# Performance work log

Hardware: AMD Instinct MI355X
Metric: run time of the kernel (lower is better)

## Reference

```python
import jax, jax.numpy as jnp
import numpy as np

WS = 8  # window_size; N = WS*WS = 64

def _rel_pos_index(ws):
    # identical to the torch buffer construction (meshgrid default 'ij')
    coords = np.stack(np.meshgrid(np.arange(ws), np.arange(ws), indexing='ij'))  # [2, ws, ws]
    cf = coords.reshape(2, -1)                       # [2, N]
    rel = cf[:, :, None] - cf[:, None, :]            # [2, N, N]
    rel = rel.transpose(1, 2, 0).astype(np.int64)    # [N, N, 2]
    rel[:, :, 0] += ws - 1
    rel[:, :, 1] += ws - 1
    rel[:, :, 0] *= 2 * ws - 1
    return jnp.asarray(rel.sum(-1), dtype=jnp.int32)  # [N, N] in [0, (2ws-1)^2)

def setup_inputs():
    key = jax.random.key(0)
    ks = jax.random.split(key, 4)
    B, N, C, H = 2048, WS * WS, 512, 16
    x = jax.random.normal(ks[0], (B, N, C), jnp.float32)
    qkv_w = jax.random.normal(ks[1], (C, 3 * C), jnp.float32) * 0.02
    proj_w = jax.random.normal(ks[2], (C, C), jnp.float32) * 0.02
    proj_b = jnp.zeros((C,), jnp.float32)
    bias_table = jax.random.normal(ks[3], ((2 * WS - 1) ** 2, H), jnp.float32) * 0.02
    rel_index = _rel_pos_index(WS)
    return {"x": x, "qkv_w": qkv_w, "proj_w": proj_w, "proj_b": proj_b,
            "bias_table": bias_table, "rel_index": rel_index}

def reference(x, qkv_w, proj_w, proj_b, bias_table, rel_index):
    B, N, C = x.shape
    H = bias_table.shape[1]
    d = C // H
    scale = d ** -0.5
    qkv = (x @ qkv_w).reshape(B, N, 3, H, d).transpose(2, 0, 3, 1, 4)  # [3,B,H,N,d]
    q, k, v = qkv[0], qkv[1], qkv[2]
    attn = jnp.einsum('bhnd,bhmd->bhnm', q, k) * scale                 # [B,H,N,N]
    bias = bias_table[rel_index.reshape(-1)].reshape(N, N, H).transpose(2, 0, 1)  # [H,N,N]
    attn = jax.nn.softmax(attn + bias[None], axis=-1)
    attn_map = attn  # dropout ratios are 0 / eval mode -> identity
    out = jnp.einsum('bhnm,bhmd->bhnd', attn, v).transpose(0, 2, 1, 3).reshape(B, N, C)
    out = out @ proj_w + proj_b
    return out, attn_map
```

## Files before the change

### kernel.cpp

```cpp
#include <hip/hip_runtime.h>
#include <cstdint>
#include <cstddef>

#define B_WIN   2048
#define N_TOK   64
#define C_DIM   512
#define H_HEADS 16
#define D_HEAD  32
#define K_DIM   512
#define M_ROWS  (B_WIN * 64)


typedef __bf16 bf16x8 __attribute__((ext_vector_type(8)));
typedef float  f32x4  __attribute__((ext_vector_type(4)));
typedef unsigned short u16x8 __attribute__((ext_vector_type(8)));

__device__ __forceinline__ unsigned short f2bf_rn(float f) {
    unsigned u = __float_as_uint(f);
    u += 0x7fffu + ((u >> 16) & 1u);
    return (unsigned short)(u >> 16);
}
__device__ __forceinline__ float bf2f(unsigned short h) {
    return __uint_as_float(((unsigned)h) << 16);
}
__device__ __forceinline__ void gload16(const void* g, void* l) {
    __builtin_amdgcn_global_load_lds(
        (const __attribute__((address_space(1))) void*)g,
        (__attribute__((address_space(3))) void*)l,
        16, 0, 0);
}

__global__ __launch_bounds__(256) void prep_kernel(
    const float* __restrict__ x,
    unsigned short* __restrict__ Xh,
    unsigned short* __restrict__ Xl,
    const float* __restrict__ qkv_w,
    unsigned short* __restrict__ qwTh,
    unsigned short* __restrict__ qwTl,
    const float* __restrict__ bias_table,
    const int* __restrict__ rel_index,
    float* __restrict__ bias_hn)
{
    const int blk = blockIdx.x;
    if (blk < 32768) {
        size_t e8 = ((size_t)blk * 256 + threadIdx.x) * 8;
        const int mb = (int)(e8 >> 16);
        const int w  = (int)(e8 & 65535);
        const int kt = w >> 12;
        const int s  = (w >> 10) & 3;
        const int r  = (w >> 3) & 127;
        const int m  = mb * 128 + r;
        const int k  = kt * 32 + s * 8;
        const float* src = &x[(size_t)m * 512 + k];
        float4 f0 = *reinterpret_cast<const float4*>(src);
        float4 f1 = *reinterpret_cast<const float4*>(src + 4);
        float fv[8] = {f0.x, f0.y, f0.z, f0.w, f1.x, f1.y, f1.z, f1.w};
        u16x8 hi, lo;
#pragma unroll
        for (int j = 0; j < 8; ++j) {
            unsigned short h = f2bf_rn(fv[j]);
            hi[j] = h;
            lo[j] = f2bf_rn(fv[j] - bf2f(h));
        }
        *reinterpret_cast<u16x8*>(&Xh[e8]) = hi;
        *reinterpret_cast<u16x8*>(&Xl[e8]) = lo;
    } else if (blk < 33152) {
        size_t e8 = ((size_t)(blk - 32768) * 256 + threadIdx.x) * 8;
        const int mb = (int)(e8 >> 16);
        const int ww = (int)(e8 & 65535);
        const int kt = ww >> 12;
        const int s  = (ww >> 10) & 3;
        const int r  = (ww >> 3) & 127;
        const int n  = mb * 128 + r;
        const int k  = kt * 32 + s * 8;
        u16x8 hi, lo;
#pragma unroll
        for (int j = 0; j < 8; ++j) {
            float v = qkv_w[(size_t)(k + j) * 1536 + n];
            unsigned short h = f2bf_rn(v);
            hi[j] = h;
            lo[j] = f2bf_rn(v - bf2f(h));
        }
        *reinterpret_cast<u16x8*>(&qwTh[e8]) = hi;
        *reinterpret_cast<u16x8*>(&qwTl[e8]) = lo;
    } else {
        int tid = (blk - 33152) * 256 + threadIdx.x;
        int h  = tid >> 12;
        int ij = tid & 4095;
        bias_hn[tid] = bias_table[rel_index[ij] * H_HEADS + h];
    }
}

__global__ __launch_bounds__(256) void wsplit_kernel(
    const float* __restrict__ w,
    unsigned short* __restrict__ wTh,
    unsigned short* __restrict__ wTl,
    int Ncols)
{
    size_t e8 = ((size_t)blockIdx.x * 256 + threadIdx.x) * 8;
    const int mb = (int)(e8 >> 16);
    const int ww = (int)(e8 & 65535);
    const int kt = ww >> 12;
    const int s  = (ww >> 10) & 3;
    const int r  = (ww >> 3) & 127;
    const int n  = mb * 128 + r;
    const int k  = kt * 32 + s * 8;
    u16x8 hi, lo;
#pragma unroll
    for (int j = 0; j < 8; ++j) {
        float v = w[(size_t)(k + j) * Ncols + n];
        unsigned short h = f2bf_rn(v);
        hi[j] = h;
        lo[j] = f2bf_rn(v - bf2f(h));
    }
    *reinterpret_cast<u16x8*>(&wTh[e8]) = hi;
    *reinterpret_cast<u16x8*>(&wTl[e8]) = lo;
}

__global__ __launch_bounds__(512, 2) void gemm_mfma_kernel(
    const unsigned short* __restrict__ ATh,
    const unsigned short* __restrict__ ATl,
    const unsigned short* __restrict__ BTh,
    const unsigned short* __restrict__ BTl,
    int mode,
    float* __restrict__ qkv_out,
    const float* __restrict__ bias,
    float* __restrict__ out,
    int Ncols_out,
    int nb_grid)
{
    extern __shared__ __align__(16) unsigned short L[];

    const int t    = threadIdx.x;
    const int lane = t & 63;
    const int wave = t >> 6;
    const int lg   = lane >> 4;
    const int lr   = lane & 15;
    const int wrow = (wave >> 2) * 128;
    const int wcol = (wave & 3) * 64;

    const int lin = blockIdx.x + gridDim.x * blockIdx.y;
    const int nwg = gridDim.x * gridDim.y;
    const int cpx = nwg >> 3;
    const int swz = (lin & 7) * cpx + (lin >> 3);
    const int m0  = (swz / nb_grid) * 256;
    const int n0  = (swz % nb_grid) * 256;
    const int mb0 = m0 >> 7;
    const int nb0 = n0 >> 7;

    f32x4 acc[8][4];
#pragma unroll
    for (int i = 0; i < 8; ++i)
#pragma unroll
        for (int j = 0; j < 4; ++j) acc[i][j] = (f32x4){0.f, 0.f, 0.f, 0.f};

    auto stage = [&](int kt, int bi) {
        const int bufbase = bi * 32768;
#pragma unroll
        for (int i = 0; i < 2; ++i) {
            const int c = i * 512 + t;
            const int r = c & 255;
            const int s = c >> 8;
            const size_t gA = (size_t)(mb0 + (r >> 7)) * 65536
                            + (size_t)kt * 4096 + s * 1024 + (r & 127) * 8;
            const size_t gB = (size_t)(nb0 + (r >> 7)) * 65536
                            + (size_t)kt * 4096 + s * 1024 + (r & 127) * 8;
            const int lo = bufbase + s * 2048 + r * 8;
            gload16(&ATh[gA], &L[lo]);
            gload16(&ATl[gA], &L[lo + 8192]);
            gload16(&BTh[gB], &L[lo + 16384]);
            gload16(&BTl[gB], &L[lo + 24576]);
        }
    };

    stage(0, 0);
    asm volatile("s_waitcnt vmcnt(0)" ::: "memory");
    __builtin_amdgcn_sched_barrier(0);
    __builtin_amdgcn_s_barrier();
    __builtin_amdgcn_sched_barrier(0);

#pragma unroll 2
    for (int ks = 0; ks < 16; ++ks) {
        const int cur = ks & 1;
        if (ks + 1 < 16) stage(ks + 1, cur ^ 1);
        const int bb = cur * 32768;

        bf16x8 bh[4], bl[4];
#pragma unroll
        for (int ni = 0; ni < 4; ++ni) {
            const int off = bb + lg * 2048 + (wcol + ni * 16 + lr) * 8;
            bh[ni] = *reinterpret_cast<const bf16x8*>(&L[off + 16384]);
            bl[ni] = *reinterpret_cast<const bf16x8*>(&L[off + 24576]);
        }
        __builtin_amdgcn_s_setprio(1);
#pragma unroll
        for (int mi = 0; mi < 8; ++mi) {
            const int aoff = bb + lg * 2048 + (wrow + mi * 16 + lr) * 8;
            bf16x8 ah = *reinterpret_cast<const bf16x8*>(&L[aoff]);
            bf16x8 al = *reinterpret_cast<const bf16x8*>(&L[aoff + 8192]);
#pragma unroll
            for (int ni = 0; ni < 4; ++ni)
                acc[mi][ni] = __builtin_amdgcn_mfma_f32_16x16x32_bf16(ah, bh[ni], acc[mi][ni], 0, 0, 0);
#pragma unroll
            for (int ni = 0; ni < 4; ++ni)
                acc[mi][ni] = __builtin_amdgcn_mfma_f32_16x16x32_bf16(ah, bl[ni], acc[mi][ni], 0, 0, 0);
#pragma unroll
            for (int ni = 0; ni < 4; ++ni)
                acc[mi][ni] = __builtin_amdgcn_mfma_f32_16x16x32_bf16(al, bh[ni], acc[mi][ni], 0, 0, 0);
        }
        __builtin_amdgcn_s_setprio(0);

        asm volatile("s_waitcnt vmcnt(0)" ::: "memory");
        __builtin_amdgcn_sched_barrier(0);
        __builtin_amdgcn_s_barrier();
        __builtin_amdgcn_sched_barrier(0);
    }

    if (mode == 0) {
#pragma unroll
        for (int mi = 0; mi < 8; ++mi)
#pragma unroll
            for (int ni = 0; ni < 4; ++ni) {
                const int col  = n0 + wcol + ni * 16 + lr;
                const int tsel = col >> 9;
                const int h    = (col >> 5) & 15;
                const int dd   = col & 31;
#pragma unroll
                for (int reg = 0; reg < 4; ++reg) {
                    const int row = m0 + wrow + mi * 16 + lg * 4 + reg;
                    const int b = row >> 6, n = row & 63;
                    qkv_out[((((size_t)tsel * B_WIN + b) * H_HEADS + h) * N_TOK + n) * D_HEAD + dd]
                        = acc[mi][ni][reg];
                }
            }
    } else {
#pragma unroll
        for (int mi = 0; mi < 8; ++mi)
#pragma unroll
            for (int ni = 0; ni < 4; ++ni) {
                const int col = n0 + wcol + ni * 16 + lr;
                const float pb = bias[col];
#pragma unroll
                for (int reg = 0; reg < 4; ++reg) {
                    const int row = m0 + wrow + mi * 16 + lg * 4 + reg;
                    out[(size_t)row * Ncols_out + col] = acc[mi][ni][reg] + pb;
                }
            }
    }
}

__global__ __launch_bounds__(256, 4) void attn_kernel(
    const float* __restrict__ qkv,
    const float* __restrict__ bias_hn,
    float* __restrict__ attn_map,
    unsigned short* __restrict__ avh,
    unsigned short* __restrict__ avl)
{
    __shared__ __align__(16) unsigned short SM[14848];
    constexpr int QH = 0, QL = 2560, KH = 5120, KL = 7680;
    constexpr int PH = 0, PL = 4608;
    constexpr int VTH = 10240, VTL = 12544;

    const int bh   = blockIdx.x;
    const int b    = bh >> 4;
    const int h    = bh & 15;
    const int t    = threadIdx.x;
    const int lane = t & 63;
    const int wv   = t >> 6;
    const int lg   = lane >> 4;
    const int lr   = lane & 15;

    const size_t plane = (size_t)B_WIN * H_HEADS * N_TOK * D_HEAD;
    const size_t base  = (size_t)bh * (N_TOK * D_HEAD);
    const float* qg = qkv + base;
    const float* kg = qkv + plane + base;
    const float* vg = qkv + 2 * plane + base;

    {
        const int r  = t >> 2;
        const int c0 = (t & 3) * 8;
        float4 a0 = *reinterpret_cast<const float4*>(&qg[r * 32 + c0]);
        float4 a1 = *reinterpret_cast<const float4*>(&qg[r * 32 + c0 + 4]);
        float qv[8] = {a0.x, a0.y, a0.z, a0.w, a1.x, a1.y, a1.z, a1.w};
        u16x8 hi, lo;
#pragma unroll
        for (int j = 0; j < 8; ++j) {
            unsigned short hh = f2bf_rn(qv[j]);
            hi[j] = hh; lo[j] = f2bf_rn(qv[j] - bf2f(hh));
        }
        *reinterpret_cast<u16x8*>(&SM[QH + r * 40 + c0]) = hi;
        *reinterpret_cast<u16x8*>(&SM[QL + r * 40 + c0]) = lo;

        float4 k0 = *reinterpret_cast<const float4*>(&kg[r * 32 + c0]);
        float4 k1 = *reinterpret_cast<const float4*>(&kg[r * 32 + c0 + 4]);
        float kv[8] = {k0.x, k0.y, k0.z, k0.w, k1.x, k1.y, k1.z, k1.w};
#pragma unroll
        for (int j = 0; j < 8; ++j) {
            unsigned short hh = f2bf_rn(kv[j]);
            hi[j] = hh; lo[j] = f2bf_rn(kv[j] - bf2f(hh));
        }
        *reinterpret_cast<u16x8*>(&SM[KH + r * 40 + c0]) = hi;
        *reinterpret_cast<u16x8*>(&SM[KL + r * 40 + c0]) = lo;

        float4 v0 = *reinterpret_cast<const float4*>(&vg[r * 32 + c0]);
        float4 v1 = *reinterpret_cast<const float4*>(&vg[r * 32 + c0 + 4]);
        float vv[8] = {v0.x, v0.y, v0.z, v0.w, v1.x, v1.y, v1.z, v1.w};
#pragma unroll
        for (int u = 0; u < 8; ++u) {
            const int d = c0 + u;
            unsigned short hh = f2bf_rn(vv[u]);
            SM[VTH + d * 72 + r] = hh;
            SM[VTL + d * 72 + r] = f2bf_rn(vv[u] - bf2f(hh));
        }
    }
    __syncthreads();

    float bias[4][4];
#pragma unroll
    for (int reg = 0; reg < 4; ++reg)
#pragma unroll
        for (int c = 0; c < 4; ++c)
            bias[reg][c] = bias_hn[(h << 12) + ((wv * 16 + lg * 4 + reg) << 6) + c * 16 + lr];

    const int ar = wv * 16 + lr;
    bf16x8 qa_h = *reinterpret_cast<const bf16x8*>(&SM[QH + ar * 40 + lg * 8]);
    bf16x8 qa_l = *reinterpret_cast<const bf16x8*>(&SM[QL + ar * 40 + lg * 8]);
    f32x4 S[4];
#pragma unroll
    for (int c = 0; c < 4; ++c) {
        const int br = c * 16 + lr;
        bf16x8 kb_h = *reinterpret_cast<const bf16x8*>(&SM[KH + br * 40 + lg * 8]);
        bf16x8 kb_l = *reinterpret_cast<const bf16x8*>(&SM[KL + br * 40 + lg * 8]);
        f32x4 s = (f32x4){0.f, 0.f, 0.f, 0.f};
        s = __builtin_amdgcn_mfma_f32_16x16x32_bf16(qa_h, kb_h, s, 0, 0, 0);
        s = __builtin_amdgcn_mfma_f32_16x16x32_bf16(qa_h, kb_l, s, 0, 0, 0);
        s = __builtin_amdgcn_mfma_f32_16x16x32_bf16(qa_l, kb_h, s, 0, 0, 0);
        S[c] = s;
    }
    __syncthreads();

    const float scale = 0.1767766952966369f;
    float p[4][4], mx[4], sm[4];
#pragma unroll
    for (int reg = 0; reg < 4; ++reg) mx[reg] = -1e30f;
#pragma unroll
    for (int reg = 0; reg < 4; ++reg)
#pragma unroll
        for (int c = 0; c < 4; ++c) {
            float s = fmaf(S[c][reg], scale, bias[reg][c]);
            p[reg][c] = s;
            mx[reg] = fmaxf(mx[reg], s);
        }
#pragma unroll
    for (int reg = 0; reg < 4; ++reg) {
        mx[reg] = fmaxf(mx[reg], __shfl_xor(mx[reg], 1));
        mx[reg] = fmaxf(mx[reg], __shfl_xor(mx[reg], 2));
        mx[reg] = fmaxf(mx[reg], __shfl_xor(mx[reg], 4));
        mx[reg] = fmaxf(mx[reg], __shfl_xor(mx[reg], 8));
        sm[reg] = 0.f;
    }
#pragma unroll
    for (int reg = 0; reg < 4; ++reg)
#pragma unroll
        for (int c = 0; c < 4; ++c) {
            float e = __expf(p[reg][c] - mx[reg]);
            p[reg][c] = e;
            sm[reg] += e;
        }
#pragma unroll
    for (int reg = 0; reg < 4; ++reg) {
        sm[reg] += __shfl_xor(sm[reg], 1);
        sm[reg] += __shfl_xor(sm[reg], 2);
        sm[reg] += __shfl_xor(sm[reg], 4);
        sm[reg] += __shfl_xor(sm[reg], 8);
        const float inv = 1.0f / sm[reg];
#pragma unroll
        for (int c = 0; c < 4; ++c) p[reg][c] *= inv;
    }

    const size_t amb = (size_t)bh * 4096;
#pragma unroll
    for (int reg = 0; reg < 4; ++reg) {
        const int R = wv * 16 + lg * 4 + reg;
#pragma unroll
        for (int c = 0; c < 4; ++c) {
            const int C = c * 16 + lr;
            const float own = p[reg][c];
            attn_map[amb + R * 64 + C] = own;
            const float mate = __shfl_xor(own, 1);
            if (!(lr & 1)) {
                unsigned short h0 = f2bf_rn(own);
                unsigned short l0 = f2bf_rn(own - bf2f(h0));
                unsigned short h1 = f2bf_rn(mate);
                unsigned short l1 = f2bf_rn(mate - bf2f(h1));
                *reinterpret_cast<unsigned*>(&SM[PH + R * 72 + C]) =
                    (unsigned)h0 | ((unsigned)h1 << 16);
                *reinterpret_cast<unsigned*>(&SM[PL + R * 72 + C]) =
                    (unsigned)l0 | ((unsigned)l1 << 16);
            }
        }
    }

    f32x4 O[2];
    O[0] = (f32x4){0.f, 0.f, 0.f, 0.f};
    O[1] = (f32x4){0.f, 0.f, 0.f, 0.f};
#pragma unroll
    for (int kk = 0; kk < 2; ++kk) {
        const int pr = wv * 16 + lr;
        bf16x8 pa_h = *reinterpret_cast<const bf16x8*>(&SM[PH + pr * 72 + kk * 32 + lg * 8]);
        bf16x8 pa_l = *reinterpret_cast<const bf16x8*>(&SM[PL + pr * 72 + kk * 32 + lg * 8]);
#pragma unroll
        for (int n = 0; n < 2; ++n) {
            const int vr = n * 16 + lr;
            bf16x8 vb_h = *reinterpret_cast<const bf16x8*>(&SM[VTH + vr * 72 + kk * 32 + lg * 8]);
            bf16x8 vb_l = *reinterpret_cast<const bf16x8*>(&SM[VTL + vr * 72 + kk * 32 + lg * 8]);
            O[n] = __builtin_amdgcn_mfma_f32_16x16x32_bf16(pa_h, vb_h, O[n], 0, 0, 0);
            O[n] = __builtin_amdgcn_mfma_f32_16x16x32_bf16(pa_h, vb_l, O[n], 0, 0, 0);
            O[n] = __builtin_amdgcn_mfma_f32_16x16x32_bf16(pa_l, vb_h, O[n], 0, 0, 0);
        }
    }

    const int mb = b >> 1;
#pragma unroll
    for (int n = 0; n < 2; ++n)
#pragma unroll
        for (int reg = 0; reg < 4; ++reg) {
            const int R  = wv * 16 + lg * 4 + reg;
            const int d  = n * 16 + lr;
            const int rl = (b & 1) * 64 + R;
            const float o = O[n][reg];
            unsigned short oh = f2bf_rn(o);
            unsigned short ol = f2bf_rn(o - bf2f(oh));
            size_t off = (size_t)mb * 65536 + (size_t)h * 4096
                       + (size_t)(d >> 3) * 1024 + (size_t)rl * 8 + (d & 7);
            avh[off] = oh;
            avl[off] = ol;
        }
}

extern "C" void kernel_launch(void* const* d_in, const int* in_sizes, int n_in,
                              void* d_out, int out_size, void* d_ws, size_t ws_size,
                              hipStream_t stream) {
    const float* x          = (const float*)d_in[0];
    const float* qkv_w      = (const float*)d_in[1];
    const float* proj_w     = (const float*)d_in[2];
    const float* proj_b     = (const float*)d_in[3];
    const float* bias_table = (const float*)d_in[4];
    const int*   rel_index  = (const int*)d_in[5];

    float* out      = (float*)d_out;
    float* attn_map = (float*)d_out + (size_t)M_ROWS * C_DIM;

    unsigned short* Xh  = (unsigned short*)d_ws;
    unsigned short* Xl  = Xh + (size_t)M_ROWS * 512;
    float*          qkv = (float*)(Xl + (size_t)M_ROWS * 512);
    unsigned short* avh = Xh;
    unsigned short* avl = Xl;

    unsigned short* qwTh = (unsigned short*)attn_map;
    unsigned short* qwTl = qwTh + (size_t)1536 * 512;
    unsigned short* pwTh = (unsigned short*)qkv;
    unsigned short* pwTl = pwTh + (size_t)512 * 512;
    float* bias_hn = out;

    prep_kernel<<<33408, 256, 0, stream>>>(
        x, Xh, Xl, qkv_w, qwTh, qwTl, bias_table, rel_index, bias_hn);
    gemm_mfma_kernel<<<dim3(6, 512), 512, 131072, stream>>>(
        Xh, Xl, qwTh, qwTl, 0, qkv, nullptr, nullptr, 1536, 6);
    attn_kernel<<<B_WIN * H_HEADS, 256, 0, stream>>>(
        qkv, bias_hn, attn_map, avh, avl);
    wsplit_kernel<<<128, 256, 0, stream>>>(proj_w, pwTh, pwTl, 512);
    gemm_mfma_kernel<<<dim3(2, 512), 512, 131072, stream>>>(
        avh, avl, pwTh, pwTl, 1, nullptr, proj_b, out, 512, 2);
}
```

Before: 1.179 ms.

## Store QKV as bf16 and drop split-precision passes in QK and projection

```diff
diff --git a/kernel.cpp b/kernel.cpp
--- a/kernel.cpp
+++ b/kernel.cpp
@@ -117,19 +117,27 @@
     *reinterpret_cast<u16x8*>(&wTl[e8]) = lo;
 }
 
+template<int NPASS>
 __global__ __launch_bounds__(512, 2) void gemm_mfma_kernel(
     const unsigned short* __restrict__ ATh,
     const unsigned short* __restrict__ ATl,
     const unsigned short* __restrict__ BTh,
     const unsigned short* __restrict__ BTl,
-    int mode,
-    float* __restrict__ qkv_out,
+    unsigned short* __restrict__ qh,
+    unsigned short* __restrict__ kh,
+    unsigned short* __restrict__ vh,
+    unsigned short* __restrict__ vl,
     const float* __restrict__ bias,
     float* __restrict__ out,
     int Ncols_out,
     int nb_grid)
 {
     extern __shared__ __align__(16) unsigned short L[];
+    constexpr int AH = 0;
+    constexpr int AL = 8192;
+    constexpr int BH = (NPASS == 3) ? 16384 : 8192;
+    constexpr int BL = (NPASS == 3) ? 24576 : 16384;
+    constexpr int STRIDE = (NPASS == 3) ? 32768 : 24576;
 
     const int t    = threadIdx.x;
     const int lane = t & 63;
@@ -155,7 +163,7 @@
         for (int j = 0; j < 4; ++j) acc[i][j] = (f32x4){0.f, 0.f, 0.f, 0.f};
 
     auto stage = [&](int kt, int bi) {
-        const int bufbase = bi * 32768;
+        const int bufbase = bi * STRIDE;
 #pragma unroll
         for (int i = 0; i < 2; ++i) {
             const int c = i * 512 + t;
@@ -166,10 +174,10 @@
             const size_t gB = (size_t)(nb0 + (r >> 7)) * 65536
                             + (size_t)kt * 4096 + s * 1024 + (r & 127) * 8;
             const int lo = bufbase + s * 2048 + r * 8;
-            gload16(&ATh[gA], &L[lo]);
-            gload16(&ATl[gA], &L[lo + 8192]);
-            gload16(&BTh[gB], &L[lo + 16384]);
-            gload16(&BTl[gB], &L[lo + 24576]);
+            gload16(&ATh[gA], &L[lo + AH]);
+            if constexpr (NPASS == 3) gload16(&ATl[gA], &L[lo + AL]);
+            gload16(&BTh[gB], &L[lo + BH]);
+            gload16(&BTl[gB], &L[lo + BL]);
         }
     };
 
@@ -183,30 +191,32 @@
     for (int ks = 0; ks < 16; ++ks) {
         const int cur = ks & 1;
         if (ks + 1 < 16) stage(ks + 1, cur ^ 1);
-        const int bb = cur * 32768;
+        const int bb = cur * STRIDE;
 
         bf16x8 bh[4], bl[4];
 #pragma unroll
         for (int ni = 0; ni < 4; ++ni) {
             const int off = bb + lg * 2048 + (wcol + ni * 16 + lr) * 8;
-            bh[ni] = *reinterpret_cast<const bf16x8*>(&L[off + 16384]);
-            bl[ni] = *reinterpret_cast<const bf16x8*>(&L[off + 24576]);
+            bh[ni] = *reinterpret_cast<const bf16x8*>(&L[off + BH]);
+            bl[ni] = *reinterpret_cast<const bf16x8*>(&L[off + BL]);
         }
         __builtin_amdgcn_s_setprio(1);
 #pragma unroll
         for (int mi = 0; mi < 8; ++mi) {
             const int aoff = bb + lg * 2048 + (wrow + mi * 16 + lr) * 8;
-            bf16x8 ah = *reinterpret_cast<const bf16x8*>(&L[aoff]);
-            bf16x8 al = *reinterpret_cast<const bf16x8*>(&L[aoff + 8192]);
+            bf16x8 ah = *reinterpret_cast<const bf16x8*>(&L[aoff + AH]);
 #pragma unroll
             for (int ni = 0; ni < 4; ++ni)
                 acc[mi][ni] = __builtin_amdgcn_mfma_f32_16x16x32_bf16(ah, bh[ni], acc[mi][ni], 0, 0, 0);
 #pragma unroll
             for (int ni = 0; ni < 4; ++ni)
                 acc[mi][ni] = __builtin_amdgcn_mfma_f32_16x16x32_bf16(ah, bl[ni], acc[mi][ni], 0, 0, 0);
-#pragma unroll
-            for (int ni = 0; ni < 4; ++ni)
-                acc[mi][ni] = __builtin_amdgcn_mfma_f32_16x16x32_bf16(al, bh[ni], acc[mi][ni], 0, 0, 0);
+            if constexpr (NPASS == 3) {
+                bf16x8 al = *reinterpret_cast<const bf16x8*>(&L[aoff + AL]);
+#pragma unroll
+                for (int ni = 0; ni < 4; ++ni)
+                    acc[mi][ni] = __builtin_amdgcn_mfma_f32_16x16x32_bf16(al, bh[ni], acc[mi][ni], 0, 0, 0);
+            }
         }
         __builtin_amdgcn_s_setprio(0);
 
@@ -216,7 +226,7 @@
         __builtin_amdgcn_sched_barrier(0);
     }
 
-    if (mode == 0) {
+    if constexpr (NPASS == 3) {
 #pragma unroll
         for (int mi = 0; mi < 8; ++mi)
 #pragma unroll
@@ -229,8 +239,17 @@
                 for (int reg = 0; reg < 4; ++reg) {
                     const int row = m0 + wrow + mi * 16 + lg * 4 + reg;
                     const int b = row >> 6, n = row & 63;
-                    qkv_out[((((size_t)tsel * B_WIN + b) * H_HEADS + h) * N_TOK + n) * D_HEAD + dd]
-                        = acc[mi][ni][reg];
+                    const size_t idx = ((((size_t)b * H_HEADS + h) * 64) + n) * 32 + dd;
+                    const float v = acc[mi][ni][reg];
+                    unsigned short hh = f2bf_rn(v);
+                    if (tsel == 0) {
+                        qh[idx] = hh;
+                    } else if (tsel == 1) {
+                        kh[idx] = hh;
+                    } else {
+                        vh[idx] = hh;
+                        vl[idx] = f2bf_rn(v - bf2f(hh));
+                    }
                 }
             }
     } else {
@@ -250,67 +269,44 @@
 }
 
 __global__ __launch_bounds__(256, 4) void attn_kernel(
-    const float* __restrict__ qkv,
+    const unsigned short* __restrict__ qh,
+    const unsigned short* __restrict__ kh,
+    const unsigned short* __restrict__ vh,
+    const unsigned short* __restrict__ vl,
     const float* __restrict__ bias_hn,
     float* __restrict__ attn_map,
-    unsigned short* __restrict__ avh,
-    unsigned short* __restrict__ avl)
+    unsigned short* __restrict__ avh)
 {
-    __shared__ __align__(16) unsigned short SM[14848];
-    constexpr int QH = 0, QL = 2560, KH = 5120, KL = 7680;
-    constexpr int PH = 0, PL = 4608;
-    constexpr int VTH = 10240, VTL = 12544;
-
-    const int bh   = blockIdx.x;
-    const int b    = bh >> 4;
-    const int h    = bh & 15;
+    __shared__ __align__(16) unsigned short SM[18944];
+    constexpr int VTH = 0, VTL = 2304;
+    constexpr int QS  = 4608, KS = 7168;
+    constexpr int PH  = 9728, PL = 14336;
+
+    const int bhid = blockIdx.x;
+    const int b    = bhid >> 4;
+    const int h    = bhid & 15;
     const int t    = threadIdx.x;
     const int lane = t & 63;
     const int wv   = t >> 6;
     const int lg   = lane >> 4;
     const int lr   = lane & 15;
 
-    const size_t plane = (size_t)B_WIN * H_HEADS * N_TOK * D_HEAD;
-    const size_t base  = (size_t)bh * (N_TOK * D_HEAD);
-    const float* qg = qkv + base;
-    const float* kg = qkv + plane + base;
-    const float* vg = qkv + 2 * plane + base;
+    const size_t base = (size_t)bhid * 2048;
 
     {
         const int r  = t >> 2;
         const int c0 = (t & 3) * 8;
-        float4 a0 = *reinterpret_cast<const float4*>(&qg[r * 32 + c0]);
-        float4 a1 = *reinterpret_cast<const float4*>(&qg[r * 32 + c0 + 4]);
-        float qv[8] = {a0.x, a0.y, a0.z, a0.w, a1.x, a1.y, a1.z, a1.w};
-        u16x8 hi, lo;
-#pragma unroll
-        for (int j = 0; j < 8; ++j) {
-            unsigned short hh = f2bf_rn(qv[j]);
-            hi[j] = hh; lo[j] = f2bf_rn(qv[j] - bf2f(hh));
-        }
-        *reinterpret_cast<u16x8*>(&SM[QH + r * 40 + c0]) = hi;
-        *reinterpret_cast<u16x8*>(&SM[QL + r * 40 + c0]) = lo;
-
-        float4 k0 = *reinterpret_cast<const float4*>(&kg[r * 32 + c0]);
-        float4 k1 = *reinterpret_cast<const float4*>(&kg[r * 32 + c0 + 4]);
-        float kv[8] = {k0.x, k0.y, k0.z, k0.w, k1.x, k1.y, k1.z, k1.w};
-#pragma unroll
-        for (int j = 0; j < 8; ++j) {
-            unsigned short hh = f2bf_rn(kv[j]);
-            hi[j] = hh; lo[j] = f2bf_rn(kv[j] - bf2f(hh));
-        }
-        *reinterpret_cast<u16x8*>(&SM[KH + r * 40 + c0]) = hi;
-        *reinterpret_cast<u16x8*>(&SM[KL + r * 40 + c0]) = lo;
-
-        float4 v0 = *reinterpret_cast<const float4*>(&vg[r * 32 + c0]);
-        float4 v1 = *reinterpret_cast<const float4*>(&vg[r * 32 + c0 + 4]);
-        float vv[8] = {v0.x, v0.y, v0.z, v0.w, v1.x, v1.y, v1.z, v1.w};
+        u16x8 q8 = *reinterpret_cast<const u16x8*>(&qh[base + r * 32 + c0]);
+        *reinterpret_cast<u16x8*>(&SM[QS + r * 40 + c0]) = q8;
+        u16x8 k8 = *reinterpret_cast<const u16x8*>(&kh[base + r * 32 + c0]);
+        *reinterpret_cast<u16x8*>(&SM[KS + r * 40 + c0]) = k8;
+        u16x8 vh8 = *reinterpret_cast<const u16x8*>(&vh[base + r * 32 + c0]);
+        u16x8 vl8 = *reinterpret_cast<const u16x8*>(&vl[base + r * 32 + c0]);
 #pragma unroll
         for (int u = 0; u < 8; ++u) {
             const int d = c0 + u;
-            unsigned short hh = f2bf_rn(vv[u]);
-            SM[VTH + d * 72 + r] = hh;
-            SM[VTL + d * 72 + r] = f2bf_rn(vv[u] - bf2f(hh));
+            SM[VTH + d * 72 + r] = vh8[u];
+            SM[VTL + d * 72 + r] = vl8[u];
         }
     }
     __syncthreads();
@@ -323,21 +319,15 @@
             bias[reg][c] = bias_hn[(h << 12) + ((wv * 16 + lg * 4 + reg) << 6) + c * 16 + lr];
 
     const int ar = wv * 16 + lr;
-    bf16x8 qa_h = *reinterpret_cast<const bf16x8*>(&SM[QH + ar * 40 + lg * 8]);
-    bf16x8 qa_l = *reinterpret_cast<const bf16x8*>(&SM[QL + ar * 40 + lg * 8]);
+    bf16x8 qa = *reinterpret_cast<const bf16x8*>(&SM[QS + ar * 40 + lg * 8]);
     f32x4 S[4];
 #pragma unroll
     for (int c = 0; c < 4; ++c) {
         const int br = c * 16 + lr;
-        bf16x8 kb_h = *reinterpret_cast<const bf16x8*>(&SM[KH + br * 40 + lg * 8]);
-        bf16x8 kb_l = *reinterpret_cast<const bf16x8*>(&SM[KL + br * 40 + lg * 8]);
+        bf16x8 kb = *reinterpret_cast<const bf16x8*>(&SM[KS + br * 40 + lg * 8]);
         f32x4 s = (f32x4){0.f, 0.f, 0.f, 0.f};
-        s = __builtin_amdgcn_mfma_f32_16x16x32_bf16(qa_h, kb_h, s, 0, 0, 0);
-        s = __builtin_amdgcn_mfma_f32_16x16x32_bf16(qa_h, kb_l, s, 0, 0, 0);
-        s = __builtin_amdgcn_mfma_f32_16x16x32_bf16(qa_l, kb_h, s, 0, 0, 0);
-        S[c] = s;
-    }
-    __syncthreads();
+        S[c] = __builtin_amdgcn_mfma_f32_16x16x32_bf16(qa, kb, s, 0, 0, 0);
+    }
 
     const float scale = 0.1767766952966369f;
     float p[4][4], mx[4], sm[4];
@@ -378,7 +368,7 @@
         for (int c = 0; c < 4; ++c) p[reg][c] *= inv;
     }
 
-    const size_t amb = (size_t)bh * 4096;
+    const size_t amb = (size_t)bhid * 4096;
 #pragma unroll
     for (int reg = 0; reg < 4; ++reg) {
         const int R = wv * 16 + lg * 4 + reg;
@@ -428,13 +418,9 @@
             const int R  = wv * 16 + lg * 4 + reg;
             const int d  = n * 16 + lr;
             const int rl = (b & 1) * 64 + R;
-            const float o = O[n][reg];
-            unsigned short oh = f2bf_rn(o);
-            unsigned short ol = f2bf_rn(o - bf2f(oh));
             size_t off = (size_t)mb * 65536 + (size_t)h * 4096
                        + (size_t)(d >> 3) * 1024 + (size_t)rl * 8 + (d & 7);
-            avh[off] = oh;
-            avl[off] = ol;
+            avh[off] = f2bf_rn(O[n][reg]);
         }
 }
 
@@ -451,25 +437,29 @@
     float* out      = (float*)d_out;
     float* attn_map = (float*)d_out + (size_t)M_ROWS * C_DIM;
 
+    const size_t PLANE = (size_t)B_WIN * H_HEADS * 64 * 32;
     unsigned short* Xh  = (unsigned short*)d_ws;
     unsigned short* Xl  = Xh + (size_t)M_ROWS * 512;
-    float*          qkv = (float*)(Xl + (size_t)M_ROWS * 512);
+    unsigned short* qhp = Xl + (size_t)M_ROWS * 512;
+    unsigned short* khp = qhp + PLANE;
+    unsigned short* vhp = khp + PLANE;
+    unsigned short* vlp = vhp + PLANE;
     unsigned short* avh = Xh;
-    unsigned short* avl = Xl;
 
     unsigned short* qwTh = (unsigned short*)attn_map;
     unsigned short* qwTl = qwTh + (size_t)1536 * 512;
-    unsigned short* pwTh = (unsigned short*)qkv;
+    unsigned short* pwTh = qhp;
     unsigned short* pwTl = pwTh + (size_t)512 * 512;
     float* bias_hn = out;
 
     prep_kernel<<<33408, 256, 0, stream>>>(
         x, Xh, Xl, qkv_w, qwTh, qwTl, bias_table, rel_index, bias_hn);
-    gemm_mfma_kernel<<<dim3(6, 512), 512, 131072, stream>>>(
-        Xh, Xl, qwTh, qwTl, 0, qkv, nullptr, nullptr, 1536, 6);
+    gemm_mfma_kernel<3><<<dim3(6, 512), 512, 131072, stream>>>(
+        Xh, Xl, qwTh, qwTl, qhp, khp, vhp, vlp, nullptr, nullptr, 1536, 6);
     attn_kernel<<<B_WIN * H_HEADS, 256, 0, stream>>>(
-        qkv, bias_hn, attn_map, avh, avl);
+        qhp, khp, vhp, vlp, bias_hn, attn_map, avh);
     wsplit_kernel<<<128, 256, 0, stream>>>(proj_w, pwTh, pwTl, 512);
-    gemm_mfma_kernel<<<dim3(2, 512), 512, 131072, stream>>>(
-        avh, avl, pwTh, pwTl, 1, nullptr, proj_b, out, 512, 2);
-}
+    gemm_mfma_kernel<2><<<dim3(2, 512), 512, 98304, stream>>>(
+        avh, nullptr, pwTh, pwTl, nullptr, nullptr, nullptr, nullptr,
+        proj_b, out, 512, 2);
+}
```

New measurement: 1.055 ms. -10.5%, faster.
